# Optimization experiments

Measured on AMD Instinct MI355X. Metric: run time of the kernel, lower is better.

## Reference

```python
import jax, jax.numpy as jnp
import numpy as np

# config (matches init_kwargs)
NA, NEN = 8, 8            # n_agents, n_enemies
NENT = NA + NEN           # n_entities
NFA, NFE = 64, 64         # state_nf_al, state_nf_en
E, A, M, HE = 64, 64, 32, 64  # entity_embed, attn_embed, mixing_embed, hypernet_embed
TD, TE = 64, 64           # task_repre_dim, task_repre_embed_dim
BS, SL = 64, 512


def setup_inputs() -> dict:
    key = jax.random.key(0)
    ks = iter(jax.random.split(key, 32))
    def rn(shape, scale=0.05):
        return jax.random.normal(next(ks), shape, dtype=jnp.float32) * scale
    return {
        "agent_qs": rn((BS, SL, NA), 1.0),
        "states": rn((BS, SL, NA * NFA + NEN * NFE), 1.0),
        "task_repre_mu": rn((BS, SL, NA, TD), 1.0),
        "ally_w": rn((NFA, E)), "ally_b": rn((E,)),
        "enemy_w": rn((NFE, E)), "enemy_b": rn((E,)),
        "q_w": rn((E, A)), "q_b": rn((A,)),
        "k_w": rn((E, A)), "k_b": rn((A,)),
        "hw1_w1": rn((E + NFA + TE, HE)), "hw1_b1": rn((HE,)),
        "hw1_w2": rn((HE, M)), "hw1_b2": rn((M,)),
        "hwf_w1": rn((E + TE, HE)), "hwf_b1": rn((HE,)),
        "hwf_w2": rn((HE, M)), "hwf_b2": rn((M,)),
        "hb1_w": rn((E + TE, M)), "hb1_b": rn((M,)),
        "v_w1": rn((E + TE, M)), "v_b1": rn((M,)),
        "v_w2": rn((M, 1)), "v_b2": rn((1,)),
        "tre_w": rn((TD, TE)), "tre_b": rn((TE,)),
    }


def reference(agent_qs, states, task_repre_mu,
              ally_w, ally_b, enemy_w, enemy_b,
              q_w, q_b, k_w, k_b,
              hw1_w1, hw1_b1, hw1_w2, hw1_b2,
              hwf_w1, hwf_b1, hwf_w2, hwf_b2,
              hb1_w, hb1_b, v_w1, v_b1, v_w2, v_b2,
              tre_w, tre_b):
    bs, sl = agent_qs.shape[:2]
    # decompose_state (state_last_action=False, state_timestep_number=False)
    ally = states[..., : NA * NFA].reshape(bs, sl, NA, NFA)      # [bs,sl,NA,NFA]
    enemy = states[..., NA * NFA:].reshape(bs, sl, NEN, NFE)     # [bs,sl,NEN,NFE]
    ally_e = ally @ ally_w + ally_b                              # [bs,sl,NA,E]
    enemy_e = enemy @ enemy_w + enemy_b                          # [bs,sl,NEN,E]
    ent = jnp.concatenate([ally_e, enemy_e], axis=2)             # [bs,sl,NENT,E]
    q = ent @ q_w + q_b                                          # [bs,sl,NENT,A]
    k = ent @ k_w + k_b
    energy = jnp.einsum('bsqa,bska->bsqk', q, k)                 # [bs,sl,NENT,NENT]
    # torch: F.softmax(energy, dim=1) on [B,n_ent,n_ent] -> softmax over query axis
    attn = jax.nn.softmax(energy, axis=2)
    # attn_out = bmm(value[B,E,n], attn[B,n,n]).mean(-1)
    attn_out = jnp.einsum('bsne,bsnk->bse', ent, attn) / NENT    # [bs,sl,E]

    mean_mu = task_repre_mu.mean(axis=-2)                        # [bs,sl,TD]
    tre = task_repre_mu @ tre_w + tre_b                          # [bs,sl,NA,TE]
    mean_tre = mean_mu @ tre_w + tre_b                           # [bs,sl,TE]

    ent_mix = jnp.concatenate([
        jnp.broadcast_to(attn_out[:, :, None, :], (bs, sl, NA, E)),
        ally, tre], axis=-1)                                     # [bs,sl,NA,E+NFA+TE]
    mix = jnp.concatenate([attn_out, mean_tre], axis=-1)         # [bs,sl,E+TE]

    w1 = jnp.abs(jax.nn.relu(ent_mix @ hw1_w1 + hw1_b1) @ hw1_w2 + hw1_b2)  # [bs,sl,NA,M]
    b1 = mix @ hb1_w + hb1_b                                     # [bs,sl,M]
    hidden = jax.nn.elu(jnp.einsum('bsn,bsnm->bsm', agent_qs, w1) + b1)     # [bs,sl,M]
    wf = jnp.abs(jax.nn.relu(mix @ hwf_w1 + hwf_b1) @ hwf_w2 + hwf_b2)      # [bs,sl,M]
    v = jax.nn.relu(mix @ v_w1 + v_b1) @ v_w2 + v_b2             # [bs,sl,1]
    q_tot = jnp.einsum('bsm,bsm->bs', hidden, wf)[..., None] + v # [bs,sl,1]
    return q_tot
```

## Files before the change

kernel.cpp:

```cpp
#include <hip/hip_runtime.h>
#include <math.h>


#define TOKS 32768

typedef __attribute__((ext_vector_type(8))) short short8;
typedef __attribute__((ext_vector_type(4))) float f32x4;

#define MFMA(a, b, c) __builtin_amdgcn_mfma_f32_16x16x32_bf16((a), (b), (c), 0, 0, 0)

#define E_CAT   0
#define E_WQKT  8192
#define E_ZBRT  13312
#define E_H1T   29696
#define E_W2T   41984
#define E_WFT   44032
#define E_BF16_TOTAL 46080
#define E_AO_US 46464

__device__ __forceinline__ unsigned short bfr(float x) {
    unsigned u = __builtin_bit_cast(unsigned, x);
    u += 0x7fffu + ((u >> 16) & 1u);
    return (unsigned short)(u >> 16);
}
__device__ __forceinline__ float bf2f(unsigned short h) {
    unsigned u = ((unsigned)h) << 16;
    return __builtin_bit_cast(float, u);
}
__device__ __forceinline__ short8 cvt8v(float4 a, float4 b) {
    short8 r;
    r[0] = (short)bfr(a.x); r[1] = (short)bfr(a.y);
    r[2] = (short)bfr(a.z); r[3] = (short)bfr(a.w);
    r[4] = (short)bfr(b.x); r[5] = (short)bfr(b.y);
    r[6] = (short)bfr(b.z); r[7] = (short)bfr(b.w);
    return r;
}
#define SWZ64(r, c)  ((((r) * 64)  + (c)) ^ (((r) & 7) << 3))
#define SWZ128(r, c) ((((r) * 128) + (c)) ^ (((r) & 7) << 3))
#define SWZ192(r, c) ((((r) * 192) + (c)) ^ (((r) & 7) << 3))

__global__ __launch_bounds__(256) void qmix_setup(
    const float* __restrict__ ally_w, const float* __restrict__ enemy_w,
    const float* __restrict__ q_w, const float* __restrict__ k_w,
    const float* __restrict__ k_b,
    const float* __restrict__ hw1_w1, const float* __restrict__ hw1_b1,
    const float* __restrict__ hw1_w2,
    const float* __restrict__ hwf_w1, const float* __restrict__ hwf_b1,
    const float* __restrict__ hwf_w2,
    const float* __restrict__ hb1_w, const float* __restrict__ hb1_b,
    const float* __restrict__ v_w1, const float* __restrict__ v_b1,
    const float* __restrict__ tre_w, const float* __restrict__ tre_b,
    unsigned short* __restrict__ wsb, float* __restrict__ wsf)
{
    int gid = blockIdx.x * 256 + threadIdx.x;
    if (gid < E_BF16_TOTAL) {
        float v = 0.f;
        int base, r, c, K;
        if (gid < E_WQKT) {
            base = E_CAT; K = 128;
            int i = gid - base; r = i >> 7; c = i & 127;
            v = (c < 64) ? ally_w[c * 64 + r] : enemy_w[(c - 64) * 64 + r];
        } else if (gid < E_ZBRT) {
            base = E_WQKT; K = 64;
            int i = gid - base; r = i >> 6; c = i & 63;
            if (r < 64) {
                for (int g = 0; g < 64; ++g) v += q_w[c * 64 + g] * k_w[r * 64 + g];
            } else if (r == 64) {
                for (int g = 0; g < 64; ++g) v += q_w[c * 64 + g] * k_b[g];
            }
        } else if (gid < E_H1T) {
            base = E_ZBRT; K = 128;
            int i = gid - base; r = i >> 7; c = i & 127;
            if (r < 64) {
                if (c < 64) v = hwf_w1[c * 64 + r];
                else for (int g = 0; g < 64; ++g) v += tre_w[(c - 64) * 64 + g] * hwf_w1[(64 + g) * 64 + r];
            } else if (r < 96) {
                int m = r - 64;
                if (c < 64) v = hb1_w[c * 32 + m];
                else for (int g = 0; g < 64; ++g) v += tre_w[(c - 64) * 64 + g] * hb1_w[(64 + g) * 32 + m];
            } else {
                int m = r - 96;
                if (c < 64) v = v_w1[c * 32 + m];
                else for (int g = 0; g < 64; ++g) v += tre_w[(c - 64) * 64 + g] * v_w1[(64 + g) * 32 + m];
            }
        } else if (gid < E_W2T) {
            base = E_H1T; K = 192;
            int i = gid - base; r = i / 192; c = i % 192;
            if (c < 64) v = hw1_w1[(64 + c) * 64 + r];
            else if (c < 128) {
                for (int g = 0; g < 64; ++g) v += tre_w[(c - 64) * 64 + g] * hw1_w1[(128 + g) * 64 + r];
            } else v = hw1_w1[(c - 128) * 64 + r];
        } else if (gid < E_WFT) {
            base = E_W2T; K = 64;
            int i = gid - base; r = i >> 6; c = i & 63;
            v = hw1_w2[c * 32 + r];
        } else {
            base = E_WFT; K = 64;
            int i = gid - base; r = i >> 6; c = i & 63;
            v = hwf_w2[c * 32 + r];
        }
        wsb[base + ((r * K + c) ^ ((r & 7) << 3))] = bfr(v);
    } else if (gid < E_BF16_TOTAL + 192) {
        int j = gid - E_BF16_TOTAL; float v;
        if (j < 64) {
            v = hw1_b1[j];
            for (int g = 0; g < 64; ++g) v += tre_b[g] * hw1_w1[(128 + g) * 64 + j];
        } else if (j < 128) {
            int e = j - 64; v = hwf_b1[e];
            for (int g = 0; g < 64; ++g) v += tre_b[g] * hwf_w1[(64 + g) * 64 + e];
        } else if (j < 160) {
            int m = j - 128; v = hb1_b[m];
            for (int g = 0; g < 64; ++g) v += tre_b[g] * hb1_w[(64 + g) * 32 + m];
        } else {
            int m = j - 160; v = v_b1[m];
            for (int g = 0; g < 64; ++g) v += tre_b[g] * v_w1[(64 + g) * 32 + m];
        }
        wsf[j] = v;
    }
}

__global__ __launch_bounds__(512) void qmix_attn(
    const float* __restrict__ states,
    const float* __restrict__ ally_b, const float* __restrict__ enemy_b,
    const unsigned short* __restrict__ wsb,
    unsigned short* __restrict__ aoG)
{
    __shared__ unsigned short sWa[13312];
    __shared__ unsigned short sE[8][1024];
    __shared__ unsigned short sT[8][1024];

    const int lane = threadIdx.x & 63;
    const int wv   = threadIdx.x >> 6;
    const int l15  = lane & 15;
    const int lg   = lane >> 4;
    const int kb   = lg * 8;
    const size_t t = (size_t)blockIdx.x * 8 + wv;

    const short8 zero8 = {0, 0, 0, 0, 0, 0, 0, 0};
    const f32x4  zero4 = {0.f, 0.f, 0.f, 0.f};

    for (int i = threadIdx.x * 8; i < 13312; i += 512 * 8)
        *(short8*)(sWa + i) = *(const short8*)(wsb + E_CAT + i);

    const int roff = (l15 < 8) ? (l15 * 64 + kb) : (512 + (l15 - 8) * 64 + kb);
    const float* p = states + t * 1024 + roff;
    float4 cur0 = *(const float4*)(p);
    float4 cur1 = *(const float4*)(p + 4);
    float4 cur2 = *(const float4*)(p + 32);
    float4 cur3 = *(const float4*)(p + 36);

    float biasEnt[4];
    #pragma unroll
    for (int nt = 0; nt < 4; ++nt) {
        int col = nt * 16 + l15;
        biasEnt[nt] = (lg < 2) ? ally_b[col] : enemy_b[col];
    }
    __syncthreads();
    const unsigned short* lCAT  = sWa;
    const unsigned short* lWQKT = sWa + 8192;

    unsigned short* E = sE[wv];
    unsigned short* T = sT[wv];

    short8 a01 = cvt8v(cur0, cur1);
    short8 a23 = cvt8v(cur2, cur3);
    const bool isally = (l15 < 8);

    f32x4 accB[4] = {zero4, zero4, zero4, zero4};
    #pragma unroll
    for (int ks = 0; ks < 4; ++ks) {
        short8 af;
        if (ks == 0)      af = isally ? a01 : zero8;
        else if (ks == 1) af = isally ? a23 : zero8;
        else if (ks == 2) af = isally ? zero8 : a01;
        else              af = isally ? zero8 : a23;
        #pragma unroll
        for (int nt = 0; nt < 4; ++nt) {
            short8 w = *(const short8*)&lCAT[SWZ128(nt * 16 + l15, ks * 32 + kb)];
            accB[nt] = MFMA(af, w, accB[nt]);
        }
    }
    float entv[4][4];
    #pragma unroll
    for (int nt = 0; nt < 4; ++nt) {
        #pragma unroll
        for (int reg = 0; reg < 4; ++reg) {
            entv[nt][reg] = accB[nt][reg] + biasEnt[nt];
            E[SWZ64(lg * 4 + reg, nt * 16 + l15)] = bfr(entv[nt][reg]);
        }
    }

    f32x4 accC[5] = {zero4, zero4, zero4, zero4, zero4};
    short8 ef0 = *(const short8*)&E[SWZ64(l15, 0 * 32 + kb)];
    short8 ef1 = *(const short8*)&E[SWZ64(l15, 1 * 32 + kb)];
    #pragma unroll
    for (int nt = 0; nt < 5; ++nt) {
        short8 w0 = *(const short8*)&lWQKT[SWZ64(nt * 16 + l15, 0 * 32 + kb)];
        short8 w1 = *(const short8*)&lWQKT[SWZ64(nt * 16 + l15, 1 * 32 + kb)];
        accC[nt] = MFMA(ef0, w0, accC[nt]);
        accC[nt] = MFMA(ef1, w1, accC[nt]);
    }
    const int src = lane & 48;
    float si[4];
    #pragma unroll
    for (int reg = 0; reg < 4; ++reg) si[reg] = __shfl(accC[4][reg], src);
    #pragma unroll
    for (int nt = 0; nt < 4; ++nt)
        #pragma unroll
        for (int reg = 0; reg < 4; ++reg)
            T[SWZ64(lg * 4 + reg, nt * 16 + l15)] = bfr(accC[nt][reg]);

    f32x4 en = zero4;
    {
        short8 ta0 = *(const short8*)&T[SWZ64(l15, 0 * 32 + kb)];
        short8 ta1 = *(const short8*)&T[SWZ64(l15, 1 * 32 + kb)];
        en = MFMA(ta0, ef0, en);
        en = MFMA(ta1, ef1, en);
    }
    #pragma unroll
    for (int reg = 0; reg < 4; ++reg) en[reg] += si[reg];

    float mx = fmaxf(fmaxf(en[0], en[1]), fmaxf(en[2], en[3]));
    mx = fmaxf(mx, __shfl_xor(mx, 16));
    mx = fmaxf(mx, __shfl_xor(mx, 32));
    float p0 = __expf(en[0] - mx), p1 = __expf(en[1] - mx);
    float p2 = __expf(en[2] - mx), p3 = __expf(en[3] - mx);
    float s = p0 + p1 + p2 + p3;
    s += __shfl_xor(s, 16);
    s += __shfl_xor(s, 32);
    float inv = 1.f / s;
    float r0 = p0 * inv, r1 = p1 * inv, r2 = p2 * inv, r3 = p3 * inv;

    float* PW = (float*)T;
    PW[(lg * 4 + 0) * 20 + l15] = r0;
    PW[(lg * 4 + 1) * 20 + l15] = r1;
    PW[(lg * 4 + 2) * 20 + l15] = r2;
    PW[(lg * 4 + 3) * 20 + l15] = r3;
    float4 q0 = *(const float4*)&PW[l15 * 20 + 0];
    float4 q1 = *(const float4*)&PW[l15 * 20 + 4];
    float4 q2 = *(const float4*)&PW[l15 * 20 + 8];
    float4 q3 = *(const float4*)&PW[l15 * 20 + 12];
    float rs_own = ((q0.x + q0.y) + (q0.z + q0.w)) + ((q1.x + q1.y) + (q1.z + q1.w))
                 + ((q2.x + q2.y) + (q2.z + q2.w)) + ((q3.x + q3.y) + (q3.z + q3.w));
    float rr[4];
    #pragma unroll
    for (int reg = 0; reg < 4; ++reg)
        rr[reg] = __shfl(rs_own, (lane & 48) | (lg * 4 + reg));

    float part[4];
    #pragma unroll
    for (int nt = 0; nt < 4; ++nt) {
        float pp = rr[0] * entv[nt][0] + rr[1] * entv[nt][1]
                 + rr[2] * entv[nt][2] + rr[3] * entv[nt][3];
        pp += __shfl_xor(pp, 16);
        pp += __shfl_xor(pp, 32);
        part[nt] = pp;
    }
    float ao = (lg == 0) ? part[0] : (lg == 1) ? part[1]
             : (lg == 2) ? part[2] : part[3];
    aoG[t * 64 + lane] = bfr(ao * 0.0625f);
}

__device__ __forceinline__ short8 mmfrag(const float* __restrict__ mp) {
    float a0 = 0.f, a1 = 0.f, a2 = 0.f, a3 = 0.f, a4 = 0.f, a5 = 0.f, a6 = 0.f, a7 = 0.f;
    #pragma unroll
    for (int a = 0; a < 8; ++a) {
        float4 u = *(const float4*)(mp + a * 64);
        float4 v = *(const float4*)(mp + a * 64 + 4);
        a0 += u.x; a1 += u.y; a2 += u.z; a3 += u.w;
        a4 += v.x; a5 += v.y; a6 += v.z; a7 += v.w;
    }
    return cvt8v(make_float4(a0 * 0.125f, a1 * 0.125f, a2 * 0.125f, a3 * 0.125f),
                 make_float4(a4 * 0.125f, a5 * 0.125f, a6 * 0.125f, a7 * 0.125f));
}

__global__ __launch_bounds__(512) void qmix_hyper(
    const float* __restrict__ agent_qs, const float* __restrict__ states,
    const float* __restrict__ mu,
    const float* __restrict__ v_w2, const float* __restrict__ v_b2,
    const float* __restrict__ hw1_b2, const float* __restrict__ hwf_b2,
    const unsigned short* __restrict__ wsb, const float* __restrict__ wsf,
    const unsigned short* __restrict__ aoG,
    float* __restrict__ out)
{
    __shared__ unsigned short sWb[16384];
    __shared__ unsigned short sMM[8192];
    __shared__ unsigned short sZT[8][1024];
    __shared__ float sB1[8][256];
    __shared__ float sWF[8][256];
    __shared__ float sV[8][8];

    const int tid  = threadIdx.x;
    const int lane = tid & 63;
    const int wv   = tid >> 6;
    const int l15  = lane & 15;
    const int lg   = lane >> 4;
    const int kb   = lg * 8;
    const int T0   = blockIdx.x * 64 + wv * 8;
    const int tokB = blockIdx.x * 64;

    const float* BH1 = wsf + 0;
    const float* BHF = wsf + 64;
    const float* BB1 = wsf + 128;
    const float* BV  = wsf + 160;

    const short8 zero8 = {0, 0, 0, 0, 0, 0, 0, 0};
    const f32x4  zero4 = {0.f, 0.f, 0.f, 0.f};

    for (int i = tid * 8; i < 16384; i += 512 * 8)
        *(short8*)(sWb + i) = *(const short8*)(wsb + E_ZBRT + i);

    short8 zA0 = *(const short8*)&aoG[(size_t)(T0 + (l15 & 7)) * 64 + kb];
    short8 zA1 = *(const short8*)&aoG[(size_t)(T0 + (l15 & 7)) * 64 + 32 + kb];

    {
        int tok = tid >> 3;
        int e8  = (tid & 7) * 8;
        const float* mp = mu + (size_t)(tokB + tok) * 512 + e8;
        float s0 = 0.f, s1 = 0.f, s2 = 0.f, s3 = 0.f,
              s4 = 0.f, s5 = 0.f, s6 = 0.f, s7 = 0.f;
        #pragma unroll
        for (int a = 0; a < 8; ++a) {
            float4 u = *(const float4*)(mp + a * 64);
            float4 v = *(const float4*)(mp + a * 64 + 4);
            s0 += u.x; s1 += u.y; s2 += u.z; s3 += u.w;
            s4 += v.x; s5 += v.y; s6 += v.z; s7 += v.w;
        }
        short8 r;
        r[0] = (short)bfr(s0 * 0.125f); r[1] = (short)bfr(s1 * 0.125f);
        r[2] = (short)bfr(s2 * 0.125f); r[3] = (short)bfr(s3 * 0.125f);
        r[4] = (short)bfr(s4 * 0.125f); r[5] = (short)bfr(s5 * 0.125f);
        r[6] = (short)bfr(s6 * 0.125f); r[7] = (short)bfr(s7 * 0.125f);
        *(short8*)&sMM[SWZ64(tok, e8)] = r;
    }
    for (int i = lane; i < 512; i += 64) sZT[wv][512 + i] = 0;
    __syncthreads();

    f32x4 zb[8] = {zero4, zero4, zero4, zero4, zero4, zero4, zero4, zero4};
    const bool arow = (l15 < 8);
    #pragma unroll
    for (int ks = 0; ks < 4; ++ks) {
        short8 af;
        if (ks == 0)      af = arow ? zA0 : zero8;
        else if (ks == 1) af = arow ? zA1 : zero8;
        else {
            short8 m = *(const short8*)&sMM[SWZ64(wv * 8 + (l15 & 7), (ks - 2) * 32 + kb)];
            af = arow ? m : zero8;
        }
        #pragma unroll
        for (int nt = 0; nt < 8; ++nt) {
            short8 w = *(const short8*)&sWb[SWZ128(nt * 16 + l15, ks * 32 + kb)];
            zb[nt] = MFMA(af, w, zb[nt]);
        }
    }
    __syncthreads();

    for (int i = tid * 8; i < 16384; i += 512 * 8)
        *(short8*)(sWb + i) = *(const short8*)(wsb + E_H1T + i);

    if (lg < 2) {
        #pragma unroll
        for (int nt = 0; nt < 4; ++nt) {
            int col = nt * 16 + l15;
            float bz = BHF[col];
            #pragma unroll
            for (int reg = 0; reg < 4; ++reg)
                sZT[wv][SWZ64(lg * 4 + reg, col)] = bfr(fmaxf(zb[nt][reg] + bz, 0.f));
        }
        #pragma unroll
        for (int nt = 4; nt < 6; ++nt) {
            int m = (nt - 4) * 16 + l15;
            float bb = BB1[m];
            #pragma unroll
            for (int reg = 0; reg < 4; ++reg)
                sB1[wv][(lg * 4 + reg) * 32 + m] = zb[nt][reg] + bb;
        }
    }
    {
        float bv0 = BV[l15], bv1 = BV[16 + l15];
        float vw0 = v_w2[l15], vw1 = v_w2[16 + l15];
        #pragma unroll
        for (int reg = 0; reg < 4; ++reg) {
            float vp = fmaxf(zb[6][reg] + bv0, 0.f) * vw0
                     + fmaxf(zb[7][reg] + bv1, 0.f) * vw1;
            vp += __shfl_xor(vp, 1); vp += __shfl_xor(vp, 2);
            vp += __shfl_xor(vp, 4); vp += __shfl_xor(vp, 8);
            if (l15 == 0 && lg < 2) sV[wv][lg * 4 + reg] = vp;
        }
    }
    __syncthreads();
    const unsigned short* lH1T = sWb;
    const unsigned short* lW2T = sWb + 12288;
    const unsigned short* lWFT = sWb + 14336;

    {
        f32x4 wfa = zero4, wfb = zero4;
        #pragma unroll
        for (int ks = 0; ks < 2; ++ks) {
            short8 af = *(const short8*)&sZT[wv][SWZ64(l15, ks * 32 + kb)];
            short8 b0 = *(const short8*)&lWFT[SWZ64(l15, ks * 32 + kb)];
            short8 b1 = *(const short8*)&lWFT[SWZ64(16 + l15, ks * 32 + kb)];
            wfa = MFMA(af, b0, wfa);
            wfb = MFMA(af, b1, wfb);
        }
        if (lg < 2) {
            float hb0 = hwf_b2[l15], hb1 = hwf_b2[16 + l15];
            #pragma unroll
            for (int reg = 0; reg < 4; ++reg) {
                int tok = lg * 4 + reg;
                sWF[wv][tok * 32 + l15]      = fabsf(wfa[reg] + hb0);
                sWF[wv][tok * 32 + 16 + l15] = fabsf(wfb[reg] + hb1);
            }
        }
    }

    const float vb2 = v_b2[0];
    const float b20 = hw1_b2[l15], b21 = hw1_b2[16 + l15];
    const int agent = l15 & 7;
    const int toff  = l15 >> 3;
    unsigned short* tile = sZT[wv];

    float4 cs0, cs1, cs2, cs3, cm0, cm1, cm2, cm3;
    short8 ca0, ca1;
    {
        const size_t tokA = (size_t)(T0 + toff);
        const float* sp = states + tokA * 1024 + agent * 64 + kb;
        const float* mp = mu + tokA * 512 + agent * 64 + kb;
        cs0 = *(const float4*)sp;        cs1 = *(const float4*)(sp + 4);
        cs2 = *(const float4*)(sp + 32); cs3 = *(const float4*)(sp + 36);
        cm0 = *(const float4*)mp;        cm1 = *(const float4*)(mp + 4);
        cm2 = *(const float4*)(mp + 32); cm3 = *(const float4*)(mp + 36);
        ca0 = *(const short8*)&aoG[tokA * 64 + kb];
        ca1 = *(const short8*)&aoG[tokA * 64 + 32 + kb];
    }

    for (int mc = 0; mc < 4; ++mc) {
        float4 us0 = cs0, us1 = cs1, us2 = cs2, us3 = cs3;
        float4 um0 = cm0, um1 = cm1, um2 = cm2, um3 = cm3;
        short8 ua0 = ca0, ua1 = ca1;
        if (mc < 3) {
            const size_t tokA = (size_t)(T0 + (mc + 1) * 2 + toff);
            const float* sp = states + tokA * 1024 + agent * 64 + kb;
            const float* mp = mu + tokA * 512 + agent * 64 + kb;
            cs0 = *(const float4*)sp;        cs1 = *(const float4*)(sp + 4);
            cs2 = *(const float4*)(sp + 32); cs3 = *(const float4*)(sp + 36);
            cm0 = *(const float4*)mp;        cm1 = *(const float4*)(mp + 4);
            cm2 = *(const float4*)(mp + 32); cm3 = *(const float4*)(mp + 36);
            ca0 = *(const short8*)&aoG[tokA * 64 + kb];
            ca1 = *(const short8*)&aoG[tokA * 64 + 32 + kb];
        }
        short8 f0 = cvt8v(us0, us1), f1 = cvt8v(us2, us3);
        short8 f2 = cvt8v(um0, um1), f3 = cvt8v(um2, um3);

        f32x4 h[4] = {zero4, zero4, zero4, zero4};
        #pragma unroll
        for (int ks = 0; ks < 6; ++ks) {
            short8 af = (ks == 0) ? f0 : (ks == 1) ? f1 : (ks == 2) ? f2
                      : (ks == 3) ? f3 : (ks == 4) ? ua0 : ua1;
            #pragma unroll
            for (int nt = 0; nt < 4; ++nt) {
                short8 w = *(const short8*)&lH1T[SWZ192(nt * 16 + l15, ks * 32 + kb)];
                h[nt] = MFMA(af, w, h[nt]);
            }
        }
        #pragma unroll
        for (int nt = 0; nt < 4; ++nt) {
            int col = nt * 16 + l15;
            float bh = BH1[col];
            #pragma unroll
            for (int reg = 0; reg < 4; ++reg)
                tile[SWZ64(lg * 4 + reg, col)] = bfr(fmaxf(h[nt][reg] + bh, 0.f));
        }

        f32x4 wa = zero4, wb = zero4;
        #pragma unroll
        for (int ks = 0; ks < 2; ++ks) {
            short8 af = *(const short8*)&tile[SWZ64(l15, ks * 32 + kb)];
            short8 b0 = *(const short8*)&lW2T[SWZ64(l15, ks * 32 + kb)];
            short8 b1 = *(const short8*)&lW2T[SWZ64(16 + l15, ks * 32 + kb)];
            wa = MFMA(af, b0, wa);
            wb = MFMA(af, b1, wb);
        }

        float hp0 = 0.f, hp1 = 0.f;
        #pragma unroll
        for (int reg = 0; reg < 4; ++reg) {
            int row = lg * 4 + reg;
            float qsv = agent_qs[(size_t)(T0 + mc * 2 + (row >> 3)) * 8 + (row & 7)];
            hp0 += qsv * fabsf(wa[reg] + b20);
            hp1 += qsv * fabsf(wb[reg] + b21);
        }
        hp0 += __shfl_xor(hp0, 16);
        hp1 += __shfl_xor(hp1, 16);
        int tokL = mc * 2 + (lg >> 1);
        float e0 = hp0 + sB1[wv][tokL * 32 + l15];
        float e1 = hp1 + sB1[wv][tokL * 32 + 16 + l15];
        float hid0 = e0 > 0.f ? e0 : (__expf(e0) - 1.f);
        float hid1 = e1 > 0.f ? e1 : (__expf(e1) - 1.f);
        float q = hid0 * sWF[wv][tokL * 32 + l15]
                + hid1 * sWF[wv][tokL * 32 + 16 + l15];
        q += __shfl_xor(q, 1); q += __shfl_xor(q, 2);
        q += __shfl_xor(q, 4); q += __shfl_xor(q, 8);
        if (l15 == 0 && (lg & 1) == 0)
            out[T0 + tokL] = q + sV[wv][tokL] + vb2;
    }
}

extern "C" void kernel_launch(void* const* d_in, const int* in_sizes, int n_in,
                              void* d_out, int out_size, void* d_ws, size_t ws_size,
                              hipStream_t stream)
{
    const float* agent_qs = (const float*)d_in[0];
    const float* states   = (const float*)d_in[1];
    const float* mu       = (const float*)d_in[2];
    const float* ally_w   = (const float*)d_in[3];
    const float* ally_b   = (const float*)d_in[4];
    const float* enemy_w  = (const float*)d_in[5];
    const float* enemy_b  = (const float*)d_in[6];
    const float* q_w      = (const float*)d_in[7];
    const float* k_w      = (const float*)d_in[9];
    const float* k_b      = (const float*)d_in[10];
    const float* hw1_w1   = (const float*)d_in[11];
    const float* hw1_b1   = (const float*)d_in[12];
    const float* hw1_w2   = (const float*)d_in[13];
    const float* hw1_b2   = (const float*)d_in[14];
    const float* hwf_w1   = (const float*)d_in[15];
    const float* hwf_b1   = (const float*)d_in[16];
    const float* hwf_w2   = (const float*)d_in[17];
    const float* hwf_b2   = (const float*)d_in[18];
    const float* hb1_w    = (const float*)d_in[19];
    const float* hb1_b    = (const float*)d_in[20];
    const float* v_w1     = (const float*)d_in[21];
    const float* v_b1     = (const float*)d_in[22];
    const float* v_w2     = (const float*)d_in[23];
    const float* v_b2     = (const float*)d_in[24];
    const float* tre_w    = (const float*)d_in[25];
    const float* tre_b    = (const float*)d_in[26];

    unsigned short* wsb = (unsigned short*)d_ws;
    float* wsf = (float*)((char*)d_ws + (size_t)E_BF16_TOTAL * 2);
    unsigned short* aoG = wsb + E_AO_US;
    float* out = (float*)d_out;

    hipLaunchKernelGGL(qmix_setup, dim3(181), dim3(256), 0, stream,
                       ally_w, enemy_w, q_w, k_w, k_b,
                       hw1_w1, hw1_b1, hw1_w2,
                       hwf_w1, hwf_b1, hwf_w2,
                       hb1_w, hb1_b, v_w1, v_b1, tre_w, tre_b,
                       wsb, wsf);

    hipLaunchKernelGGL(qmix_attn, dim3(TOKS / 8), dim3(512), 0, stream,
                       states, ally_b, enemy_b, wsb, aoG);

    hipLaunchKernelGGL(qmix_hyper, dim3(TOKS / 64), dim3(512), 0, stream,
                       agent_qs, states, mu, v_w2, v_b2, hw1_b2, hwf_b2,
                       wsb, wsf, aoG, out);
}
```

Baseline: 87.31 us.

## Software-pipeline hypernet w1 chunks, overlapping next H1 MFMAs with previous epilogue

Restructures the per-wave mixing loop into a software pipeline. The first-layer H1 MFMAs for chunk mc are issued alongside the second-layer W2 MFMAs and epilogue of chunk mc-1, and there is a prologue and a tail. The aim is to hide the LDS tile round-trip latency and dependency stalls between the two MFMA stages. It keeps the h accumulators of one chunk live alongside the previous chunk's work, which raises register pressure, and it fully unrolls the loop.

Result: slower. 90.32 us (+3.4%).

```diff
diff --git a/kernel.cpp b/kernel.cpp
--- a/kernel.cpp
+++ b/kernel.cpp
@@ -420,6 +420,56 @@
     const int toff  = l15 >> 3;
     unsigned short* tile = sZT[wv];
 
+    auto EPI = [&](int c, const f32x4& wa, const f32x4& wb) {
+        float hp0 = 0.f, hp1 = 0.f;
+        #pragma unroll
+        for (int reg = 0; reg < 4; ++reg) {
+            int row = lg * 4 + reg;
+            float qsv = agent_qs[(size_t)(T0 + c * 2 + (row >> 3)) * 8 + (row & 7)];
+            hp0 += qsv * fabsf(wa[reg] + b20);
+            hp1 += qsv * fabsf(wb[reg] + b21);
+        }
+        hp0 += __shfl_xor(hp0, 16);
+        hp1 += __shfl_xor(hp1, 16);
+        int tokL = c * 2 + (lg >> 1);
+        float e0 = hp0 + sB1[wv][tokL * 32 + l15];
+        float e1 = hp1 + sB1[wv][tokL * 32 + 16 + l15];
+        float hid0 = e0 > 0.f ? e0 : (__expf(e0) - 1.f);
+        float hid1 = e1 > 0.f ? e1 : (__expf(e1) - 1.f);
+        float q = hid0 * sWF[wv][tokL * 32 + l15]
+                + hid1 * sWF[wv][tokL * 32 + 16 + l15];
+        q += __shfl_xor(q, 1); q += __shfl_xor(q, 2);
+        q += __shfl_xor(q, 4); q += __shfl_xor(q, 8);
+        if (l15 == 0 && (lg & 1) == 0)
+            out[T0 + tokL] = q + sV[wv][tokL] + vb2;
+    };
+    auto H1C = [&](float4 u0, float4 u1, float4 u2, float4 u3,
+                   float4 m0, float4 m1, float4 m2, float4 m3,
+                   short8 a0, short8 a1, f32x4* h) {
+        short8 f0 = cvt8v(u0, u1), f1 = cvt8v(u2, u3);
+        short8 f2 = cvt8v(m0, m1), f3 = cvt8v(m2, m3);
+        #pragma unroll
+        for (int ks = 0; ks < 6; ++ks) {
+            short8 af = (ks == 0) ? f0 : (ks == 1) ? f1 : (ks == 2) ? f2
+                      : (ks == 3) ? f3 : (ks == 4) ? a0 : a1;
+            #pragma unroll
+            for (int nt = 0; nt < 4; ++nt) {
+                short8 w = *(const short8*)&lH1T[SWZ192(nt * 16 + l15, ks * 32 + kb)];
+                h[nt] = MFMA(af, w, h[nt]);
+            }
+        }
+    };
+    auto TILEW = [&](const f32x4* h) {
+        #pragma unroll
+        for (int nt = 0; nt < 4; ++nt) {
+            int col = nt * 16 + l15;
+            float bh = BH1[col];
+            #pragma unroll
+            for (int reg = 0; reg < 4; ++reg)
+                tile[SWZ64(lg * 4 + reg, col)] = bfr(fmaxf(h[nt][reg] + bh, 0.f));
+        }
+    };
+
     float4 cs0, cs1, cs2, cs3, cm0, cm1, cm2, cm3;
     short8 ca0, ca1;
     {
@@ -433,11 +483,31 @@
         ca0 = *(const short8*)&aoG[tokA * 64 + kb];
         ca1 = *(const short8*)&aoG[tokA * 64 + 32 + kb];
     }
-
-    for (int mc = 0; mc < 4; ++mc) {
-        float4 us0 = cs0, us1 = cs1, us2 = cs2, us3 = cs3;
-        float4 um0 = cm0, um1 = cm1, um2 = cm2, um3 = cm3;
-        short8 ua0 = ca0, ua1 = ca1;
+    {
+        float4 u0 = cs0, u1 = cs1, u2 = cs2, u3 = cs3;
+        float4 m0 = cm0, m1 = cm1, m2 = cm2, m3 = cm3;
+        short8 a0 = ca0, a1 = ca1;
+        {
+            const size_t tokA = (size_t)(T0 + 2 + toff);
+            const float* sp = states + tokA * 1024 + agent * 64 + kb;
+            const float* mp = mu + tokA * 512 + agent * 64 + kb;
+            cs0 = *(const float4*)sp;        cs1 = *(const float4*)(sp + 4);
+            cs2 = *(const float4*)(sp + 32); cs3 = *(const float4*)(sp + 36);
+            cm0 = *(const float4*)mp;        cm1 = *(const float4*)(mp + 4);
+            cm2 = *(const float4*)(mp + 32); cm3 = *(const float4*)(mp + 36);
+            ca0 = *(const short8*)&aoG[tokA * 64 + kb];
+            ca1 = *(const short8*)&aoG[tokA * 64 + 32 + kb];
+        }
+        f32x4 h[4] = {zero4, zero4, zero4, zero4};
+        H1C(u0, u1, u2, u3, m0, m1, m2, m3, a0, a1, h);
+        TILEW(h);
+    }
+
+    #pragma unroll
+    for (int mc = 1; mc < 4; ++mc) {
+        float4 u0 = cs0, u1 = cs1, u2 = cs2, u3 = cs3;
+        float4 m0 = cm0, m1 = cm1, m2 = cm2, m3 = cm3;
+        short8 a0 = ca0, a1 = ca1;
         if (mc < 3) {
             const size_t tokA = (size_t)(T0 + (mc + 1) * 2 + toff);
             const float* sp = states + tokA * 1024 + agent * 64 + kb;
@@ -449,60 +519,33 @@
             ca0 = *(const short8*)&aoG[tokA * 64 + kb];
             ca1 = *(const short8*)&aoG[tokA * 64 + 32 + kb];
         }
-        short8 f0 = cvt8v(us0, us1), f1 = cvt8v(us2, us3);
-        short8 f2 = cvt8v(um0, um1), f3 = cvt8v(um2, um3);
-
+        short8 afw0 = *(const short8*)&tile[SWZ64(l15, 0 * 32 + kb)];
+        short8 afw1 = *(const short8*)&tile[SWZ64(l15, 1 * 32 + kb)];
         f32x4 h[4] = {zero4, zero4, zero4, zero4};
-        #pragma unroll
-        for (int ks = 0; ks < 6; ++ks) {
-            short8 af = (ks == 0) ? f0 : (ks == 1) ? f1 : (ks == 2) ? f2
-                      : (ks == 3) ? f3 : (ks == 4) ? ua0 : ua1;
-            #pragma unroll
-            for (int nt = 0; nt < 4; ++nt) {
-                short8 w = *(const short8*)&lH1T[SWZ192(nt * 16 + l15, ks * 32 + kb)];
-                h[nt] = MFMA(af, w, h[nt]);
-            }
-        }
-        #pragma unroll
-        for (int nt = 0; nt < 4; ++nt) {
-            int col = nt * 16 + l15;
-            float bh = BH1[col];
-            #pragma unroll
-            for (int reg = 0; reg < 4; ++reg)
-                tile[SWZ64(lg * 4 + reg, col)] = bfr(fmaxf(h[nt][reg] + bh, 0.f));
-        }
-
+        H1C(u0, u1, u2, u3, m0, m1, m2, m3, a0, a1, h);
         f32x4 wa = zero4, wb = zero4;
-        #pragma unroll
-        for (int ks = 0; ks < 2; ++ks) {
-            short8 af = *(const short8*)&tile[SWZ64(l15, ks * 32 + kb)];
-            short8 b0 = *(const short8*)&lW2T[SWZ64(l15, ks * 32 + kb)];
-            short8 b1 = *(const short8*)&lW2T[SWZ64(16 + l15, ks * 32 + kb)];
-            wa = MFMA(af, b0, wa);
-            wb = MFMA(af, b1, wb);
-        }
-
-        float hp0 = 0.f, hp1 = 0.f;
-        #pragma unroll
-        for (int reg = 0; reg < 4; ++reg) {
-            int row = lg * 4 + reg;
-            float qsv = agent_qs[(size_t)(T0 + mc * 2 + (row >> 3)) * 8 + (row & 7)];
-            hp0 += qsv * fabsf(wa[reg] + b20);
-            hp1 += qsv * fabsf(wb[reg] + b21);
-        }
-        hp0 += __shfl_xor(hp0, 16);
-        hp1 += __shfl_xor(hp1, 16);
-        int tokL = mc * 2 + (lg >> 1);
-        float e0 = hp0 + sB1[wv][tokL * 32 + l15];
-        float e1 = hp1 + sB1[wv][tokL * 32 + 16 + l15];
-        float hid0 = e0 > 0.f ? e0 : (__expf(e0) - 1.f);
-        float hid1 = e1 > 0.f ? e1 : (__expf(e1) - 1.f);
-        float q = hid0 * sWF[wv][tokL * 32 + l15]
-                + hid1 * sWF[wv][tokL * 32 + 16 + l15];
-        q += __shfl_xor(q, 1); q += __shfl_xor(q, 2);
-        q += __shfl_xor(q, 4); q += __shfl_xor(q, 8);
-        if (l15 == 0 && (lg & 1) == 0)
-            out[T0 + tokL] = q + sV[wv][tokL] + vb2;
+        {
+            short8 b00 = *(const short8*)&lW2T[SWZ64(l15, 0 * 32 + kb)];
+            short8 b01 = *(const short8*)&lW2T[SWZ64(l15, 1 * 32 + kb)];
+            short8 b10 = *(const short8*)&lW2T[SWZ64(16 + l15, 0 * 32 + kb)];
+            short8 b11 = *(const short8*)&lW2T[SWZ64(16 + l15, 1 * 32 + kb)];
+            wa = MFMA(afw0, b00, wa); wa = MFMA(afw1, b01, wa);
+            wb = MFMA(afw0, b10, wb); wb = MFMA(afw1, b11, wb);
+        }
+        EPI(mc - 1, wa, wb);
+        TILEW(h);
+    }
+    {
+        short8 afw0 = *(const short8*)&tile[SWZ64(l15, 0 * 32 + kb)];
+        short8 afw1 = *(const short8*)&tile[SWZ64(l15, 1 * 32 + kb)];
+        f32x4 wa = zero4, wb = zero4;
+        short8 b00 = *(const short8*)&lW2T[SWZ64(l15, 0 * 32 + kb)];
+        short8 b01 = *(const short8*)&lW2T[SWZ64(l15, 1 * 32 + kb)];
+        short8 b10 = *(const short8*)&lW2T[SWZ64(16 + l15, 0 * 32 + kb)];
+        short8 b11 = *(const short8*)&lW2T[SWZ64(16 + l15, 1 * 32 + kb)];
+        wa = MFMA(afw0, b00, wa); wa = MFMA(afw1, b01, wa);
+        wb = MFMA(afw0, b10, wb); wb = MFMA(afw1, b11, wb);
+        EPI(3, wa, wb);
     }
 }
 
```
